# Kernel optimization log

Hardware: AMD Instinct MI355X
Metric: run time of the kernel (lower is better)

The kernel has to match this reference:

```python
import jax, jax.numpy as jnp
import numpy as np

N_LOC, N_EVT, E = 100000, 200000, 1000000
F_LOC, F_EVT, H = 128, 128, 64


def setup_inputs() -> dict:
    key = jax.random.key(0)
    ks = jax.random.split(key, 12)
    s = lambda k, shp: jax.random.normal(k, shp, dtype=jnp.float32) * (1.0 / np.sqrt(shp[0]))
    return {
        "loc_x": jax.random.normal(ks[0], (N_LOC, F_LOC), dtype=jnp.float32),
        "evt_x": jax.random.normal(ks[1], (N_EVT, F_EVT), dtype=jnp.float32),
        "edge_index": jax.random.randint(ks[2], (2, E), 0, N_LOC, dtype=jnp.int64),
        # projections (stored as (in, out))
        "W_loc": s(ks[3], (F_LOC, H)), "b_loc": jnp.zeros((H,), jnp.float32),
        "W_evt": s(ks[4], (F_EVT, H)), "b_evt": jnp.zeros((H,), jnp.float32),
        # SAGEConv: lin_l (on aggregated src, with bias), lin_r (on dst root, no bias)
        "W_l": s(ks[5], (H, H)), "b_l": jnp.zeros((H,), jnp.float32),
        "W_r": s(ks[6], (H, H)),
        # head MLP
        "W_h1": s(ks[7], (H, H // 2)), "b_h1": jnp.zeros((H // 2,), jnp.float32),
        "W_h2": s(ks[8], (H // 2, 1)), "b_h2": jnp.zeros((1,), jnp.float32),
    }


def reference(loc_x, evt_x, edge_index, W_loc, b_loc, W_evt, b_evt,
              W_l, b_l, W_r, W_h1, b_h1, W_h2, b_h2):
    # node projections + ReLU
    loc_h = jax.nn.relu(loc_x @ W_loc + b_loc)   # [N_loc, H]
    evt_h = jax.nn.relu(evt_x @ W_evt + b_evt)   # [N_evt, H]

    src, dst = edge_index[0], edge_index[1]      # event -> location
    n_loc = loc_h.shape[0]
    # mean aggregation of source (event) features onto destination (location) nodes
    msg_sum = jax.ops.segment_sum(evt_h[src], dst, num_segments=n_loc)   # [N_loc, H]
    cnt = jax.ops.segment_sum(jnp.ones_like(dst, dtype=loc_h.dtype), dst,
                              num_segments=n_loc)
    agg = msg_sum / jnp.maximum(cnt, 1.0)[:, None]
    # SAGEConv: lin_l(agg) + lin_r(root), then ReLU
    loc_h = jax.nn.relu(agg @ W_l + b_l + loc_h @ W_r)

    # prediction head
    h = jax.nn.relu(loc_h @ W_h1 + b_h1)
    logits = (h @ W_h2 + b_h2)[:, 0]             # [N_loc]
    return logits
```

## Files before the change

### kernel.cpp

```cpp
#include <hip/hip_runtime.h>


#define N_LOC 100000
#define N_EVT 200000
#define E_CNT 1000000
#define NTILES 6250
#define NBKT   256
#define BKT_L  391
#define CAPG   6000
#define QCAP   32
#define PERB   7813

typedef __attribute__((ext_vector_type(8))) short short8;
typedef __attribute__((ext_vector_type(4))) float floatx4;

__device__ __forceinline__ float b2f(unsigned short u) {
    unsigned int x = ((unsigned int)u) << 16;
    return __builtin_bit_cast(float, x);
}
__device__ __forceinline__ unsigned short f2b(float f) {
    unsigned int x = __builtin_bit_cast(unsigned int, f);
    unsigned int r = (x + 0x7fffu + ((x >> 16) & 1u)) >> 16;
    return (unsigned short)r;
}
__device__ __forceinline__ float loadf(const void* p, int f32, size_t i) {
    return f32 ? ((const float*)p)[i] : b2f(((const unsigned short*)p)[i]);
}

__global__ __launch_bounds__(256) void prep_kernel(
    const void* t0, const void* t1, const int* eidx,
    const void* t3, const void* t4, const void* t5, const void* t6,
    const void* t7, const void* t8, const void* t9, const void* t10,
    const void* t11, const void* t12, const void* t13,
    int* flags, int* gbc, unsigned short* __restrict__ wp_all) {
    int b = blockIdx.x, tid = threadIdx.x;
    __shared__ int s0, s1;

    if (b == 14) { gbc[tid] = 0; return; }

    if (b >= 15) {
        int pb = b - 15;
        const void* W; int K, N, bstart, off;
        if (pb < 4)       { W = t5;  K = 128; N = 64; bstart = 0;  off = 0; }
        else if (pb < 8)  { W = t3;  K = 128; N = 64; bstart = 4;  off = 8192; }
        else if (pb < 10) { W = t7;  K = 64;  N = 64; bstart = 8;  off = 16384; }
        else if (pb < 12) { W = t9;  K = 64;  N = 64; bstart = 10; off = 20480; }
        else              { W = t10; K = 64;  N = 32; bstart = 12; off = 24576; }
        if (tid == 0) s0 = 0;
        __syncthreads();
        int nsamp = 2 * K * N; if (nsamp > 1024) nsamp = 1024;
        const unsigned short* h = (const unsigned short*)W;
        int susp = 0;
        for (int i = tid; i < nsamp; i += 256)
            if (((h[i] >> 7) & 0xFF) >= 0x90) susp++;
        if (susp) atomicAdd(&s0, susp);
        __syncthreads();
        int f32 = (s0 * 16 >= nsamp) ? 1 : 0;

        int idx  = (pb - bstart) * 256 + tid;
        int nk   = K >> 5;
        int f    = idx >> 6;
        int lane = idx & 63;
        int t  = f / nk;
        int kk = f - t * nk;
        int n  = t * 16 + (lane & 15);
        int k0 = kk * 32 + (lane >> 4) * 8;
        unsigned short tmp[8];
#pragma unroll
        for (int j = 0; j < 8; ++j) {
            size_t src = (size_t)(k0 + j) * N + n;
            tmp[j] = f32 ? f2b(((const float*)W)[src])
                         : ((const unsigned short*)W)[src];
        }
#pragma unroll
        for (int j = 0; j < 8; ++j) wp_all[(size_t)off + (size_t)idx * 8 + j] = tmp[j];
        return;
    }

    if (tid == 0) { s0 = 0; s1 = 0; }
    __syncthreads();
    if (b == 13) {
        if (tid < 128) {
            if (eidx[2 * tid] != 0) atomicAdd(&s0, 1);
            if (eidx[2 * tid + 1] != 0) atomicAdd(&s1, 1);
        }
        __syncthreads();
        if (tid == 0) flags[2] = (s1 == 0 && s0 > 32) ? 1 : 0;
        return;
    }
    const void* ptrs[13] = {t0, t1, t3, t4, t5, t6, t7, t8, t9, t10, t11, t12, t13};
    const int   cnts[13] = {12800000, 25600000, 8192, 64, 8192, 64,
                            4096, 64, 4096, 2048, 32, 32, 1};
    const int   slot[13] = {0, 1, 3, 4, 5, 6, 7, 8, 9, 10, 11, 12, 13};
    int nsamp = 2 * cnts[b];
    if (nsamp > 1024) nsamp = 1024;
    const unsigned short* h = (const unsigned short*)ptrs[b];
    int susp = 0;
    for (int i = tid; i < nsamp; i += 256)
        if (((h[i] >> 7) & 0xFF) >= 0x90) susp++;
    if (susp) atomicAdd(&s0, susp);
    __syncthreads();
    if (tid == 0) flags[slot[b]] = (s0 * 16 >= nsamp) ? 1 : 0;
}

__global__ __launch_bounds__(256) void proj_both_kernel(
    const void* __restrict__ evt_x, const void* __restrict__ loc_x,
    const unsigned short* __restrict__ wp_all,
    const void* __restrict__ b_evt, const void* __restrict__ b_loc,
    unsigned short* __restrict__ evt_h, unsigned short* __restrict__ loc_h,
    const int* __restrict__ flags) {
    int blk = blockIdx.x;
    const void* X; const unsigned short* Wp; const void* bias;
    unsigned short* Y; int M, fx, fb, bb;
    if (blk < 3125) { X = evt_x; Wp = wp_all;        bias = b_evt; Y = evt_h;
                      M = N_EVT; fx = flags[1]; fb = flags[6]; bb = blk; }
    else            { X = loc_x; Wp = wp_all + 8192; bias = b_loc; Y = loc_h;
                      M = N_LOC; fx = flags[0]; fb = flags[4]; bb = blk - 3125; }
    int tid  = threadIdx.x;
    int lane = tid & 63;
    int wv   = tid >> 6;
    int l15  = lane & 15;
    int quad = lane >> 4;
    int row_base = bb * 64 + wv * 16;

    short8 b[16];
#pragma unroll
    for (int f = 0; f < 16; ++f)
        b[f] = *reinterpret_cast<const short8*>(Wp + ((size_t)(f * 64 + lane)) * 8);

    int m = row_base + l15;
    short8 a[4];
#pragma unroll
    for (int kk = 0; kk < 4; ++kk) a[kk] = (short8)0;
    if (m < M) {
        if (fx) {
            const float* xr = (const float*)X + (size_t)m * 128 + quad * 8;
#pragma unroll
            for (int kk = 0; kk < 4; ++kk) {
                float4 p0 = *reinterpret_cast<const float4*>(xr + kk * 32);
                float4 p1 = *reinterpret_cast<const float4*>(xr + kk * 32 + 4);
                short8 v;
                v[0] = (short)f2b(p0.x); v[1] = (short)f2b(p0.y);
                v[2] = (short)f2b(p0.z); v[3] = (short)f2b(p0.w);
                v[4] = (short)f2b(p1.x); v[5] = (short)f2b(p1.y);
                v[6] = (short)f2b(p1.z); v[7] = (short)f2b(p1.w);
                a[kk] = v;
            }
        } else {
            const unsigned short* xr = (const unsigned short*)X + (size_t)m * 128 + quad * 8;
#pragma unroll
            for (int kk = 0; kk < 4; ++kk)
                a[kk] = *reinterpret_cast<const short8*>(xr + kk * 32);
        }
    }

    floatx4 acc[4];
#pragma unroll
    for (int t = 0; t < 4; ++t) acc[t] = (floatx4)0.0f;
#pragma unroll
    for (int kk = 0; kk < 4; ++kk) {
#pragma unroll
        for (int t = 0; t < 4; ++t)
            acc[t] = __builtin_amdgcn_mfma_f32_16x16x32_bf16(
                a[kk], b[t * 4 + kk], acc[t], 0, 0, 0);
    }

#pragma unroll
    for (int t = 0; t < 4; ++t) {
        float bv = loadf(bias, fb, t * 16 + l15);
#pragma unroll
        for (int r = 0; r < 4; ++r) {
            int row = row_base + quad * 4 + r;
            if (row < M) {
                float v = acc[t][r] + bv;
                v = v > 0.0f ? v : 0.0f;
                Y[(size_t)row * 64 + t * 16 + l15] = f2b(v);
            }
        }
    }
}

__global__ __launch_bounds__(256) void bucket_kernel(
    const int* __restrict__ eidx, uint2* __restrict__ bkt,
    int* __restrict__ gbc, const int* __restrict__ flags) {
    __shared__ uint2 queue[NBKT][QCAP];
    __shared__ int qcnt[NBKT];
    int tid = threadIdx.x, blk = blockIdx.x;
    qcnt[tid] = 0;
    __syncthreads();
    int f64 = flags[2];
    const long long* e64 = (const long long*)eidx;
    int e0 = blk * PERB;
    int e1 = e0 + PERB; if (e1 > E_CNT) e1 = E_CNT;
    const int rounds = (PERB + 255) / 256;

    for (int r = 0; r < rounds; ++r) {
        int e = e0 + r * 256 + tid;
        if (e < e1) {
            int src, dst;
            if (f64) { src = (int)e64[e]; dst = (int)e64[E_CNT + e]; }
            else     { src = eidx[e];     dst = eidx[E_CNT + e]; }
            if ((unsigned)dst < (unsigned)N_LOC && (unsigned)src < (unsigned)N_EVT) {
                int bk = dst / BKT_L;
                int pos = atomicAdd(&qcnt[bk], 1);
                if (pos < QCAP) {
                    queue[bk][pos] = make_uint2((unsigned)src, (unsigned)dst);
                } else {
                    int p = atomicAdd(&gbc[bk], 1);
                    if (p < CAPG) bkt[(size_t)bk * CAPG + p] = make_uint2(src, dst);
                }
            }
        }
        __syncthreads();
        int n = qcnt[tid]; if (n > QCAP) n = QCAP;
        while (n >= 16) {
            int gp = atomicAdd(&gbc[tid], 16);
            if (gp + 16 <= CAPG) {
                uint2* d = bkt + (size_t)tid * CAPG + gp;
#pragma unroll
                for (int j = 0; j < 16; ++j) d[j] = queue[tid][j];
            }
#pragma unroll
            for (int j = 16; j < QCAP; ++j) queue[tid][j - 16] = queue[tid][j];
            n -= 16;
        }
        qcnt[tid] = n;
        __syncthreads();
    }
    int n = qcnt[tid]; if (n > QCAP) n = QCAP;
    if (n > 0) {
        int gp = atomicAdd(&gbc[tid], n);
        for (int j = 0; j < n; ++j)
            if (gp + j < CAPG) bkt[(size_t)tid * CAPG + gp + j] = queue[tid][j];
    }
}

__global__ void scan_gbc_kernel(const int* __restrict__ gbc,
                                int* __restrict__ bbase) {
    __shared__ int sh[256];
    int t = threadIdx.x;
    int v = gbc[t]; if (v > CAPG) v = CAPG;
    sh[t] = v;
    __syncthreads();
    for (int d = 1; d < 256; d <<= 1) {
        int x = (t >= d) ? sh[t - d] : 0;
        __syncthreads();
        sh[t] += x;
        __syncthreads();
    }
    bbase[t] = sh[t] - v;
}

__global__ __launch_bounds__(256) void csr_build_kernel(
    const uint2* __restrict__ bkt, const int* __restrict__ gbc,
    const int* __restrict__ bbase,
    int* __restrict__ rowptr, int* __restrict__ csr) {
    __shared__ int lcnt[512];
    __shared__ int lscan[512];
    __shared__ int lcsr[CAPG];
    int b = blockIdx.x, tid = threadIdx.x;
    int loc0 = b * BKT_L;
    int nloc = N_LOC - loc0; if (nloc > BKT_L) nloc = BKT_L;
    int cntE = gbc[b]; if (cntE > CAPG) cntE = CAPG;
    int base = bbase[b];
    const uint2* bp = bkt + (size_t)b * CAPG;

    int i0 = tid, i1 = tid + 256;
    lcnt[i0] = 0; lcnt[i1] = 0;
    __syncthreads();
    for (int i = tid; i < cntE; i += 256) {
        int d = (int)bp[i].y - loc0;
        atomicAdd(&lcnt[d], 1);
    }
    __syncthreads();
    lscan[i0] = lcnt[i0]; lscan[i1] = lcnt[i1];
    __syncthreads();
    for (int d = 1; d < 512; d <<= 1) {
        int v0 = (i0 >= d) ? lscan[i0 - d] : 0;
        int v1 = (i1 >= d) ? lscan[i1 - d] : 0;
        __syncthreads();
        lscan[i0] += v0; lscan[i1] += v1;
        __syncthreads();
    }
    for (int i = tid; i < nloc; i += 256) {
        int excl = lscan[i] - lcnt[i];
        rowptr[loc0 + i] = base + excl;
        lcnt[i] = excl;
    }
    if (b == NBKT - 1 && tid == 0) rowptr[N_LOC] = base + cntE;
    __syncthreads();
    for (int i = tid; i < cntE; i += 256) {
        uint2 pr = bp[i];
        int d = (int)pr.y - loc0;
        int p = atomicAdd(&lcnt[d], 1);
        if (p < CAPG) lcsr[p] = (int)pr.x;
    }
    __syncthreads();
    for (int i = tid; i < cntE; i += 256) csr[base + i] = lcsr[i];
}

__global__ __launch_bounds__(256) void aggregate_kernel(
    const unsigned short* __restrict__ evt_h,
    const int* __restrict__ rowptr, const int* __restrict__ csr,
    unsigned short* __restrict__ agg, int N) {
    int wid  = (blockIdx.x * 256 + threadIdx.x) >> 6;
    int lane = threadIdx.x & 63;
    if (wid >= N) return;
    int e0 = rowptr[wid], e1 = rowptr[wid + 1];
    float acc = 0.0f;
    for (int j = e0; j < e1; j += 4) {
        int c1 = j + 1 < e1, c2 = j + 2 < e1, c3 = j + 3 < e1;
        int s0 = csr[j];
        int s1 = csr[c1 ? j + 1 : j];
        int s2 = csr[c2 ? j + 2 : j];
        int s3 = csr[c3 ? j + 3 : j];
        float v0 = b2f(evt_h[(size_t)s0 * 64 + lane]);
        float v1 = b2f(evt_h[(size_t)s1 * 64 + lane]);
        float v2 = b2f(evt_h[(size_t)s2 * 64 + lane]);
        float v3 = b2f(evt_h[(size_t)s3 * 64 + lane]);
        acc += v0;
        if (c1) acc += v1;
        if (c2) acc += v2;
        if (c3) acc += v3;
    }
    float inv = (e1 > e0) ? 1.0f / (float)(e1 - e0) : 0.0f;
    agg[(size_t)wid * 64 + lane] = f2b(acc * inv);
}

__global__ __launch_bounds__(256) void head_kernel(
    const unsigned short* __restrict__ agg,
    const unsigned short* __restrict__ loc_h,
    const unsigned short* __restrict__ wp_all,
    const void* __restrict__ bl, const void* __restrict__ bh1,
    const void* __restrict__ wh2, const void* __restrict__ bh2,
    void* __restrict__ out, const int* __restrict__ flags) {
    __shared__ unsigned short h2s[4][16 * 64];
    int tid = threadIdx.x, lane = tid & 63, wv = tid >> 6;
    int tile = blockIdx.x * 4 + wv;
    if (tile >= NTILES) return;
    int l15 = lane & 15, quad = lane >> 4;
    int fbl = flags[8], fbh1 = flags[11], fwh2 = flags[12], fbh2 = flags[13];
    int fout = flags[0];
    int base = tile * 16;
    const unsigned short* wp_l  = wp_all + 16384;
    const unsigned short* wp_r  = wp_all + 20480;
    const unsigned short* wp_h1 = wp_all + 24576;

    short8 bwl[8], bwr[8], bw1[4];
#pragma unroll
    for (int f = 0; f < 8; ++f) {
        bwl[f] = *reinterpret_cast<const short8*>(wp_l + ((size_t)(f * 64 + lane)) * 8);
        bwr[f] = *reinterpret_cast<const short8*>(wp_r + ((size_t)(f * 64 + lane)) * 8);
    }
#pragma unroll
    for (int f = 0; f < 4; ++f)
        bw1[f] = *reinterpret_cast<const short8*>(wp_h1 + ((size_t)(f * 64 + lane)) * 8);

    short8 aA[2], aL[2];
#pragma unroll
    for (int kk = 0; kk < 2; ++kk) {
        aA[kk] = *reinterpret_cast<const short8*>(
            agg + (size_t)(base + l15) * 64 + kk * 32 + quad * 8);
        aL[kk] = *reinterpret_cast<const short8*>(
            loc_h + (size_t)(base + l15) * 64 + kk * 32 + quad * 8);
    }

    floatx4 acc[4];
#pragma unroll
    for (int t = 0; t < 4; ++t) acc[t] = (floatx4)0.0f;
#pragma unroll
    for (int kk = 0; kk < 2; ++kk) {
#pragma unroll
        for (int t = 0; t < 4; ++t) {
            acc[t] = __builtin_amdgcn_mfma_f32_16x16x32_bf16(
                aA[kk], bwl[t * 2 + kk], acc[t], 0, 0, 0);
            acc[t] = __builtin_amdgcn_mfma_f32_16x16x32_bf16(
                aL[kk], bwr[t * 2 + kk], acc[t], 0, 0, 0);
        }
    }

#pragma unroll
    for (int t = 0; t < 4; ++t) {
        float bb = loadf(bl, fbl, t * 16 + l15);
#pragma unroll
        for (int r = 0; r < 4; ++r) {
            float v = acc[t][r] + bb;
            v = v > 0.0f ? v : 0.0f;
            h2s[wv][(quad * 4 + r) * 64 + t * 16 + l15] = f2b(v);
        }
    }
    short8 aH[2];
#pragma unroll
    for (int kk = 0; kk < 2; ++kk)
        aH[kk] = *reinterpret_cast<const short8*>(
            &h2s[wv][l15 * 64 + kk * 32 + quad * 8]);

    floatx4 a1[2];
#pragma unroll
    for (int t = 0; t < 2; ++t) a1[t] = (floatx4)0.0f;
#pragma unroll
    for (int kk = 0; kk < 2; ++kk)
#pragma unroll
        for (int t = 0; t < 2; ++t)
            a1[t] = __builtin_amdgcn_mfma_f32_16x16x32_bf16(
                aH[kk], bw1[t * 2 + kk], a1[t], 0, 0, 0);

    float s[4] = {0.f, 0.f, 0.f, 0.f};
#pragma unroll
    for (int t = 0; t < 2; ++t) {
        float bb = loadf(bh1, fbh1, t * 16 + l15);
        float w2 = loadf(wh2, fwh2, t * 16 + l15);
#pragma unroll
        for (int r = 0; r < 4; ++r) {
            float v = a1[t][r] + bb;
            v = v > 0.0f ? v : 0.0f;
            s[r] += v * w2;
        }
    }
#pragma unroll
    for (int r = 0; r < 4; ++r) {
        s[r] += __shfl_xor(s[r], 1);
        s[r] += __shfl_xor(s[r], 2);
        s[r] += __shfl_xor(s[r], 4);
        s[r] += __shfl_xor(s[r], 8);
    }
    float bb2 = loadf(bh2, fbh2, 0);
#pragma unroll
    for (int r = 0; r < 4; ++r) {
        if (l15 == r) {
            int row = base + quad * 4 + r;
            float v = s[r] + bb2;
            if (fout) ((float*)out)[row] = v;
            else      ((unsigned short*)out)[row] = f2b(v);
        }
    }
}

extern "C" void kernel_launch(void* const* d_in, const int* in_sizes, int n_in,
                              void* d_out, int out_size, void* d_ws, size_t ws_size,
                              hipStream_t stream) {
    (void)in_sizes; (void)n_in; (void)out_size; (void)ws_size;
    const void* loc_x = d_in[0];
    const void* evt_x = d_in[1];
    const int*  eidx  = (const int*)d_in[2];
    const void* W_loc = d_in[3];
    const void* b_loc = d_in[4];
    const void* W_evt = d_in[5];
    const void* b_evt = d_in[6];
    const void* W_l   = d_in[7];
    const void* b_l   = d_in[8];
    const void* W_r   = d_in[9];
    const void* W_h1  = d_in[10];
    const void* b_h1  = d_in[11];
    const void* W_h2  = d_in[12];
    const void* b_h2  = d_in[13];

    char* ws = (char*)d_ws;
    unsigned short* evt_h  = (unsigned short*)(ws);
    unsigned short* loc_h  = (unsigned short*)(ws + 25600000);
    int*            csr    = (int*)(ws + 38400000);
    int*            rowptr = (int*)(ws + 42400000);
    int*            gbc    = (int*)(ws + 42800016);
    int*            bbase  = (int*)(ws + 42801040);
    unsigned short* wp_all = (unsigned short*)(ws + 42802064);
    int*            flags  = (int*)(ws + 42855312);
    uint2*          bkt    = (uint2*)(ws + 42855376);
    unsigned short* agg    = (unsigned short*)(ws + 42855376);

    prep_kernel<<<28, 256, 0, stream>>>(
        loc_x, evt_x, eidx, W_loc, b_loc, W_evt, b_evt,
        W_l, b_l, W_r, W_h1, b_h1, W_h2, b_h2,
        flags, gbc, wp_all);

    proj_both_kernel<<<4688, 256, 0, stream>>>(evt_x, loc_x, wp_all,
                                               b_evt, b_loc, evt_h, loc_h, flags);

    bucket_kernel<<<128, 256, 0, stream>>>(eidx, bkt, gbc, flags);
    scan_gbc_kernel<<<1, 256, 0, stream>>>(gbc, bbase);
    csr_build_kernel<<<NBKT, 256, 0, stream>>>(bkt, gbc, bbase, rowptr, csr);

    aggregate_kernel<<<(N_LOC + 3) / 4, 256, 0, stream>>>(evt_h, rowptr, csr,
                                                          agg, N_LOC);

    head_kernel<<<(NTILES + 3) / 4, 256, 0, stream>>>(
        agg, loc_h, wp_all, b_l, b_h1, W_h2, b_h2, d_out, flags);
}
```

Baseline: 349.2 us.

## Make projection kernel persistent with grid-stride strips and prefetched A fragments

```diff
diff --git a/kernel.cpp b/kernel.cpp
--- a/kernel.cpp
+++ b/kernel.cpp
@@ -10,6 +10,9 @@
 #define CAPG   6000
 #define QCAP   32
 #define PERB   7813
+
+#define PROJ_EVT_BLK 768
+#define PROJ_LOC_BLK 384
 
 typedef __attribute__((ext_vector_type(8))) short short8;
 typedef __attribute__((ext_vector_type(4))) float floatx4;
@@ -103,6 +106,29 @@
     if (tid == 0) flags[slot[b]] = (s0 * 16 >= nsamp) ? 1 : 0;
 }
 
+__device__ __forceinline__ void load_a_frags(
+    const void* __restrict__ X, int fx, int m, int quad, short8* a) {
+    if (fx) {
+        const float* xr = (const float*)X + (size_t)m * 128 + quad * 8;
+#pragma unroll
+        for (int kk = 0; kk < 4; ++kk) {
+            float4 p0 = *reinterpret_cast<const float4*>(xr + kk * 32);
+            float4 p1 = *reinterpret_cast<const float4*>(xr + kk * 32 + 4);
+            short8 v;
+            v[0] = (short)f2b(p0.x); v[1] = (short)f2b(p0.y);
+            v[2] = (short)f2b(p0.z); v[3] = (short)f2b(p0.w);
+            v[4] = (short)f2b(p1.x); v[5] = (short)f2b(p1.y);
+            v[6] = (short)f2b(p1.z); v[7] = (short)f2b(p1.w);
+            a[kk] = v;
+        }
+    } else {
+        const unsigned short* xr = (const unsigned short*)X + (size_t)m * 128 + quad * 8;
+#pragma unroll
+        for (int kk = 0; kk < 4; ++kk)
+            a[kk] = *reinterpret_cast<const short8*>(xr + kk * 32);
+    }
+}
+
 __global__ __launch_bounds__(256) void proj_both_kernel(
     const void* __restrict__ evt_x, const void* __restrict__ loc_x,
     const unsigned short* __restrict__ wp_all,
@@ -110,73 +136,65 @@
     unsigned short* __restrict__ evt_h, unsigned short* __restrict__ loc_h,
     const int* __restrict__ flags) {
     int blk = blockIdx.x;
-    const void* X; const unsigned short* Wp; const void* bias;
-    unsigned short* Y; int M, fx, fb, bb;
-    if (blk < 3125) { X = evt_x; Wp = wp_all;        bias = b_evt; Y = evt_h;
-                      M = N_EVT; fx = flags[1]; fb = flags[6]; bb = blk; }
-    else            { X = loc_x; Wp = wp_all + 8192; bias = b_loc; Y = loc_h;
-                      M = N_LOC; fx = flags[0]; fb = flags[4]; bb = blk - 3125; }
     int tid  = threadIdx.x;
     int lane = tid & 63;
     int wv   = tid >> 6;
     int l15  = lane & 15;
     int quad = lane >> 4;
-    int row_base = bb * 64 + wv * 16;
+
+    const void* X; const unsigned short* Wp; const void* bias;
+    unsigned short* Y; int fx, fb, wid, nwaves, nstrips;
+    if (blk < PROJ_EVT_BLK) {
+        X = evt_x; Wp = wp_all;        bias = b_evt; Y = evt_h;
+        fx = flags[1]; fb = flags[6];
+        wid = blk * 4 + wv; nwaves = PROJ_EVT_BLK * 4; nstrips = N_EVT / 16;
+    } else {
+        X = loc_x; Wp = wp_all + 8192; bias = b_loc; Y = loc_h;
+        fx = flags[0]; fb = flags[4];
+        wid = (blk - PROJ_EVT_BLK) * 4 + wv; nwaves = PROJ_LOC_BLK * 4;
+        nstrips = N_LOC / 16;
+    }
 
     short8 b[16];
 #pragma unroll
     for (int f = 0; f < 16; ++f)
         b[f] = *reinterpret_cast<const short8*>(Wp + ((size_t)(f * 64 + lane)) * 8);
-
-    int m = row_base + l15;
-    short8 a[4];
-#pragma unroll
-    for (int kk = 0; kk < 4; ++kk) a[kk] = (short8)0;
-    if (m < M) {
-        if (fx) {
-            const float* xr = (const float*)X + (size_t)m * 128 + quad * 8;
-#pragma unroll
-            for (int kk = 0; kk < 4; ++kk) {
-                float4 p0 = *reinterpret_cast<const float4*>(xr + kk * 32);
-                float4 p1 = *reinterpret_cast<const float4*>(xr + kk * 32 + 4);
-                short8 v;
-                v[0] = (short)f2b(p0.x); v[1] = (short)f2b(p0.y);
-                v[2] = (short)f2b(p0.z); v[3] = (short)f2b(p0.w);
-                v[4] = (short)f2b(p1.x); v[5] = (short)f2b(p1.y);
-                v[6] = (short)f2b(p1.z); v[7] = (short)f2b(p1.w);
-                a[kk] = v;
+    float bv[4];
+#pragma unroll
+    for (int t = 0; t < 4; ++t) bv[t] = loadf(bias, fb, t * 16 + l15);
+
+    int s = wid;
+    if (s >= nstrips) return;
+    short8 a[4], a2[4];
+    load_a_frags(X, fx, s * 16 + l15, quad, a);
+
+    for (; s < nstrips; s += nwaves) {
+        int sn = s + nwaves;
+        if (sn < nstrips) load_a_frags(X, fx, sn * 16 + l15, quad, a2);
+
+        floatx4 acc[4];
+#pragma unroll
+        for (int t = 0; t < 4; ++t) acc[t] = (floatx4)0.0f;
+#pragma unroll
+        for (int kk = 0; kk < 4; ++kk) {
+#pragma unroll
+            for (int t = 0; t < 4; ++t)
+                acc[t] = __builtin_amdgcn_mfma_f32_16x16x32_bf16(
+                    a[kk], b[t * 4 + kk], acc[t], 0, 0, 0);
+        }
+
+        int row_base = s * 16;
+#pragma unroll
+        for (int t = 0; t < 4; ++t) {
+#pragma unroll
+            for (int r = 0; r < 4; ++r) {
+                float v = acc[t][r] + bv[t];
+                v = v > 0.0f ? v : 0.0f;
+                Y[(size_t)(row_base + quad * 4 + r) * 64 + t * 16 + l15] = f2b(v);
             }
-        } else {
-            const unsigned short* xr = (const unsigned short*)X + (size_t)m * 128 + quad * 8;
-#pragma unroll
-            for (int kk = 0; kk < 4; ++kk)
-                a[kk] = *reinterpret_cast<const short8*>(xr + kk * 32);
-        }
-    }
-
-    floatx4 acc[4];
-#pragma unroll
-    for (int t = 0; t < 4; ++t) acc[t] = (floatx4)0.0f;
-#pragma unroll
-    for (int kk = 0; kk < 4; ++kk) {
-#pragma unroll
-        for (int t = 0; t < 4; ++t)
-            acc[t] = __builtin_amdgcn_mfma_f32_16x16x32_bf16(
-                a[kk], b[t * 4 + kk], acc[t], 0, 0, 0);
-    }
-
-#pragma unroll
-    for (int t = 0; t < 4; ++t) {
-        float bv = loadf(bias, fb, t * 16 + l15);
-#pragma unroll
-        for (int r = 0; r < 4; ++r) {
-            int row = row_base + quad * 4 + r;
-            if (row < M) {
-                float v = acc[t][r] + bv;
-                v = v > 0.0f ? v : 0.0f;
-                Y[(size_t)row * 64 + t * 16 + l15] = f2b(v);
-            }
-        }
+        }
+#pragma unroll
+        for (int kk = 0; kk < 4; ++kk) a[kk] = a2[kk];
     }
 }
 
@@ -472,8 +490,8 @@
         W_l, b_l, W_r, W_h1, b_h1, W_h2, b_h2,
         flags, gbc, wp_all);
 
-    proj_both_kernel<<<4688, 256, 0, stream>>>(evt_x, loc_x, wp_all,
-                                               b_evt, b_loc, evt_h, loc_h, flags);
+    proj_both_kernel<<<PROJ_EVT_BLK + PROJ_LOC_BLK, 256, 0, stream>>>(
+        evt_x, loc_x, wp_all, b_evt, b_loc, evt_h, loc_h, flags);
 
     bucket_kernel<<<128, 256, 0, stream>>>(eidx, bkt, gbc, flags);
     scan_gbc_kernel<<<1, 256, 0, stream>>>(gbc, bbase);
```

New measurement: 353.3 us. Within noise of the previous version (+1.2%).
